# Performance work log

Hardware: AMD Instinct MI355X
Metric: run time of the kernel (lower is better)

## Reference

```python
import jax, jax.numpy as jnp
import numpy as np

N = 100000   # nodes
E = 1600000  # edges
C = 128      # channels
EPS = 1e-5   # BatchNorm eps (PyG gnn.BatchNorm default)


def gcn_conv(x, W, b, src, dst, n):
    """PyG GCNConv: linear -> sym-normalized aggregation with self-loops -> bias."""
    h = x @ W                                      # [N, C]
    # degree with self-loops: in-degree at dst + 1
    deg = jnp.zeros((n,), h.dtype).at[dst].add(jnp.ones((), h.dtype)) + 1.0
    dinv = jax.lax.rsqrt(deg)                      # [N]
    norm = dinv[src] * dinv[dst]                   # [E]
    agg = jnp.zeros_like(h).at[dst].add(h[src] * norm[:, None])
    agg = agg + h * (dinv * dinv)[:, None]         # self-loop contribution
    return agg + b


def batch_norm(x, gamma, beta):
    """Training-mode BatchNorm over the node dimension (per-channel)."""
    mu = jnp.mean(x, axis=0)
    var = jnp.mean(jnp.square(x - mu), axis=0)     # biased variance
    return (x - mu) * jax.lax.rsqrt(var + EPS) * gamma + beta


def setup_inputs() -> dict:
    key = jax.random.key(0)
    ks = jax.random.split(key, 8)
    s = 1.0 / np.sqrt(C)
    x = jax.random.normal(ks[0], (N, C), dtype=jnp.float32)
    edge_index = jax.random.randint(ks[1], (2, E), 0, N, dtype=jnp.int64)
    W1 = jax.random.uniform(ks[2], (C, C), jnp.float32, -s, s)
    b1 = jax.random.uniform(ks[3], (C,), jnp.float32, -s, s)
    W2 = jax.random.uniform(ks[4], (C, C), jnp.float32, -s, s)
    b2 = jax.random.uniform(ks[5], (C,), jnp.float32, -s, s)
    gamma2 = jnp.ones((C,), jnp.float32)
    beta2 = jnp.zeros((C,), jnp.float32)
    return {"x": x, "W1": W1, "b1": b1, "W2": W2, "b2": b2,
            "gamma2": gamma2, "beta2": beta2, "edge_index": edge_index}


def reference(x, W1, b1, W2, b2, gamma2, beta2, edge_index):
    src, dst = edge_index[0], edge_index[1]
    identity = x
    # NOTE: original forward applies batch_norm2 after BOTH convs (batch_norm1 unused).
    h = jax.nn.relu(batch_norm(gcn_conv(x, W1, b1, src, dst, N), gamma2, beta2))
    h = batch_norm(gcn_conv(h, W2, b2, src, dst, N), gamma2, beta2)
    return jax.nn.relu(h + identity)
```

## Files before the change

kernel.cpp:

```cpp
#include <hip/hip_runtime.h>

#define N_NODES 100000
#define EDGES   1600000
#define CH      128
#define BN_EPS  1e-5f

#define BINS     782
#define CHUNKS   256
#define CHUNK_E  (EDGES / CHUNKS)
#define HM       (BINS * CHUNKS)
#define SCAN_NB  (HM / 256)
#define NREP     64

typedef __attribute__((ext_vector_type(8))) __bf16 bf16x8;
typedef __attribute__((ext_vector_type(4))) __bf16 bf16x4;
typedef __attribute__((ext_vector_type(2))) __bf16 bf16x2;
typedef __attribute__((ext_vector_type(4))) float  f32x4;

__global__ __launch_bounds__(256) void histo_kernel(const int* __restrict__ dst,
                                                    int* __restrict__ histo_g) {
    __shared__ int h[BINS];
    int t = threadIdx.x;
    for (int b = t; b < BINS; b += 256) h[b] = 0;
    __syncthreads();
    int base = blockIdx.x * CHUNK_E;
    for (int i = t; i < CHUNK_E; i += 256)
        atomicAdd(&h[dst[base + i] >> 7], 1);
    __syncthreads();
    for (int b = t; b < BINS; b += 256)
        histo_g[b * CHUNKS + blockIdx.x] = h[b];
}

__global__ __launch_bounds__(256) void scan1(const int* __restrict__ in,
                                             int* __restrict__ scanned,
                                             int* __restrict__ blocksum) {
    __shared__ int sh[2][256];
    int t = threadIdx.x;
    int i = blockIdx.x * 256 + t;
    int v = in[i];
    sh[0][t] = v;
    __syncthreads();
    int pp = 0;
    #pragma unroll
    for (int off = 1; off < 256; off <<= 1) {
        int val = sh[pp][t] + ((t >= off) ? sh[pp][t - off] : 0);
        sh[1 - pp][t] = val;
        pp = 1 - pp;
        __syncthreads();
    }
    int incl = sh[pp][t];
    scanned[i] = incl - v;
    if (t == 255) blocksum[blockIdx.x] = incl;
}

__global__ __launch_bounds__(1024) void scan2(int* __restrict__ blocksum) {
    __shared__ int sh[2][1024];
    int t = threadIdx.x;
    int v = (t < SCAN_NB) ? blocksum[t] : 0;
    sh[0][t] = v;
    __syncthreads();
    int pp = 0;
    #pragma unroll
    for (int off = 1; off < 1024; off <<= 1) {
        int val = sh[pp][t] + ((t >= off) ? sh[pp][t - off] : 0);
        sh[1 - pp][t] = val;
        pp = 1 - pp;
        __syncthreads();
    }
    if (t < SCAN_NB) blocksum[t] = sh[pp][t] - v;
}

__global__ __launch_bounds__(256) void place_kernel(const int* __restrict__ src,
                                                    const int* __restrict__ dst,
                                                    const int* __restrict__ scanned,
                                                    const int* __restrict__ blocksum,
                                                    int* __restrict__ binned) {
    __shared__ int cur[BINS];
    int t = threadIdx.x;
    for (int b = t; b < BINS; b += 256)
        cur[b] = scanned[b * CHUNKS + blockIdx.x] + blocksum[b];
    __syncthreads();
    int base = blockIdx.x * CHUNK_E;
    for (int i = t; i < CHUNK_E; i += 256) {
        int d = dst[base + i];
        int s = src[base + i];
        int pos = atomicAdd(&cur[d >> 7], 1);
        binned[pos] = (s << 7) | (d & 127);
    }
}

__global__ __launch_bounds__(256) void bin_csr(const int* __restrict__ binned,
                                               const int* __restrict__ scanned,
                                               const int* __restrict__ blocksum,
                                               int* __restrict__ srcs,
                                               int* __restrict__ rowptr,
                                               float* __restrict__ dinv) {
    __shared__ int cnt[128];
    __shared__ int sc[2][128];
    __shared__ int base[128];
    __shared__ int cur[128];
    const int t = threadIdx.x;
    const int bin = blockIdx.x;
    if (t < 128) { cnt[t] = 0; cur[t] = 0; }
    __syncthreads();
    const int beg = scanned[bin * CHUNKS] + blocksum[bin];
    const int end = (bin == BINS - 1) ? EDGES
                    : (scanned[(bin + 1) * CHUNKS] + blocksum[bin + 1]);
    for (int e = beg + t; e < end; e += 256)
        atomicAdd(&cnt[binned[e] & 127], 1);
    __syncthreads();
    if (t < 128) sc[0][t] = cnt[t];
    __syncthreads();
    int pp = 0;
    #pragma unroll
    for (int off = 1; off < 128; off <<= 1) {
        if (t < 128) sc[1 - pp][t] = sc[pp][t] + ((t >= off) ? sc[pp][t - off] : 0);
        pp = 1 - pp;
        __syncthreads();
    }
    if (t < 128) {
        base[t] = beg + sc[pp][t] - cnt[t];
        int n = (bin << 7) + t;
        if (n < N_NODES) {
            rowptr[n] = base[t];
            dinv[n] = rsqrtf((float)cnt[t] + 1.0f);
        }
    }
    if (bin == 0 && t == 0) rowptr[N_NODES] = EDGES;
    __syncthreads();
    for (int e = beg + t; e < end; e += 256) {
        int p = binned[e];
        int dl = p & 127;
        int pos = base[dl] + atomicAdd(&cur[dl], 1);
        srcs[pos] = p >> 7;
    }
}

__global__ __launch_bounds__(256) void wtrans2(const float* __restrict__ W1,
                                               __bf16* __restrict__ Wt1,
                                               const float* __restrict__ W2,
                                               __bf16* __restrict__ Wt2,
                                               unsigned* __restrict__ hspad) {
    int b = blockIdx.x;
    if (b == 0 && threadIdx.x < 64) hspad[threadIdx.x] = 0u;
    const float* W = (b < 64) ? W1 : W2;
    __bf16* Wt = (b < 64) ? Wt1 : Wt2;
    int idx = (b & 63) * 256 + threadIdx.x;
    int n = idx >> 7, k = idx & 127;
    Wt[idx] = (__bf16)W[k * 128 + n];
}

__global__ __launch_bounds__(256) void gemm_f32(const float* __restrict__ A,
                                                const __bf16* __restrict__ Wt,
                                                const float* __restrict__ dinv,
                                                __bf16* __restrict__ hs) {
    const int wave = threadIdx.x >> 6;
    const int rt = blockIdx.x * 4 + wave;
    if (rt >= N_NODES / 16) return;
    const int lane = threadIdx.x & 63;
    const int ln = lane & 15;
    const int quad = lane >> 4;
    const int arow = rt * 16 + ln;

    f32x4 acc[8];
    #pragma unroll
    for (int ct = 0; ct < 8; ++ct) acc[ct] = (f32x4){0.f, 0.f, 0.f, 0.f};

    #pragma unroll
    for (int k0 = 0; k0 < 128; k0 += 32) {
        const int k = k0 + quad * 8;
        float4 a0 = *(const float4*)(A + (size_t)arow * CH + k);
        float4 a1 = *(const float4*)(A + (size_t)arow * CH + k + 4);
        bf16x8 af;
        af[0] = (__bf16)a0.x; af[1] = (__bf16)a0.y;
        af[2] = (__bf16)a0.z; af[3] = (__bf16)a0.w;
        af[4] = (__bf16)a1.x; af[5] = (__bf16)a1.y;
        af[6] = (__bf16)a1.z; af[7] = (__bf16)a1.w;
        #pragma unroll
        for (int ct = 0; ct < 8; ++ct) {
            bf16x8 bfrag = *(const bf16x8*)(Wt + (size_t)(ct * 16 + ln) * CH + k);
            acc[ct] = __builtin_amdgcn_mfma_f32_16x16x32_bf16(af, bfrag, acc[ct], 0, 0, 0);
        }
    }

    #pragma unroll
    for (int r = 0; r < 4; ++r) {
        const int row_r = rt * 16 + quad * 4 + r;
        const float dr = dinv[row_r];
        __bf16* orow = hs + (size_t)row_r * CH + ln;
        #pragma unroll
        for (int ct = 0; ct < 8; ++ct)
            orow[ct * 16] = (__bf16)(acc[ct][r] * dr);
    }
}

__global__ __launch_bounds__(256) void gemm_bn(const __bf16* __restrict__ A,
                                               const __bf16* __restrict__ Wt,
                                               const float* __restrict__ dinv,
                                               const float* __restrict__ scale,
                                               const float* __restrict__ shift,
                                               __bf16* __restrict__ hs) {
    const int wave = threadIdx.x >> 6;
    const int rt = blockIdx.x * 4 + wave;
    if (rt >= N_NODES / 16) return;
    const int lane = threadIdx.x & 63;
    const int ln = lane & 15;
    const int quad = lane >> 4;
    const int arow = rt * 16 + ln;

    f32x4 acc[8];
    #pragma unroll
    for (int ct = 0; ct < 8; ++ct) acc[ct] = (f32x4){0.f, 0.f, 0.f, 0.f};

    #pragma unroll
    for (int k0 = 0; k0 < 128; k0 += 32) {
        const int k = k0 + quad * 8;
        bf16x8 av = *(const bf16x8*)(A + (size_t)arow * CH + k);
        bf16x8 af;
        #pragma unroll
        for (int j = 0; j < 8; ++j)
            af[j] = (__bf16)fmaxf(fmaf((float)av[j], scale[k + j], shift[k + j]), 0.f);
        #pragma unroll
        for (int ct = 0; ct < 8; ++ct) {
            bf16x8 bfrag = *(const bf16x8*)(Wt + (size_t)(ct * 16 + ln) * CH + k);
            acc[ct] = __builtin_amdgcn_mfma_f32_16x16x32_bf16(af, bfrag, acc[ct], 0, 0, 0);
        }
    }

    #pragma unroll
    for (int r = 0; r < 4; ++r) {
        const int row_r = rt * 16 + quad * 4 + r;
        const float dr = dinv[row_r];
        __bf16* orow = hs + (size_t)row_r * CH + ln;
        #pragma unroll
        for (int ct = 0; ct < 8; ++ct)
            orow[ct * 16] = (__bf16)(acc[ct][r] * dr);
    }
}

__global__ __launch_bounds__(256) void gather_agg(const __bf16* __restrict__ hs,
                                                  const int* __restrict__ srcs,
                                                  const int* __restrict__ rowptr,
                                                  const float* __restrict__ dinv,
                                                  __bf16* __restrict__ agg,
                                                  float* __restrict__ gpart) {
    __shared__ float red[4][64][4];
    const int wave = threadIdx.x >> 6;
    const int c2 = threadIdx.x & 63;
    const bf16x2* hp = (const bf16x2*)hs;

    const int n0 = __builtin_amdgcn_readfirstlane(blockIdx.x * 8 + wave * 2);
    const int n1 = n0 + 1;
    const int b0 = rowptr[n0];
    const int e0 = rowptr[n0 + 1];
    const int e1 = rowptr[n1 + 1];
    const int b1 = e0;
    const int d0 = e0 - b0, d1 = e1 - b1;
    const int nt = (max(d0, d1) + 7) >> 3;

    bf16x2 sv0 = hp[(size_t)n0 * 64 + c2];
    bf16x2 sv1 = hp[(size_t)n1 * 64 + c2];
    float ax0 = (float)sv0[0], ay0 = (float)sv0[1];
    float ax1 = (float)sv1[0], ay1 = (float)sv1[1];

    int j0 = b0, j1 = b1;
    for (int t = 0; t < nt; ++t) {
        int ea[8], eb[8];
        #pragma unroll
        for (int u = 0; u < 8; ++u) {
            int sa = srcs[j0 + u];
            int sb = srcs[j1 + u];
            ea[u] = (j0 + u < e0) ? sa : N_NODES;
            eb[u] = (j1 + u < e1) ? sb : N_NODES;
        }
        bf16x2 va[8], vb[8];
        #pragma unroll
        for (int u = 0; u < 8; ++u) va[u] = hp[(size_t)ea[u] * 64 + c2];
        #pragma unroll
        for (int u = 0; u < 8; ++u) vb[u] = hp[(size_t)eb[u] * 64 + c2];
        ax0 += (((float)va[0][0] + (float)va[1][0]) + ((float)va[2][0] + (float)va[3][0]))
             + (((float)va[4][0] + (float)va[5][0]) + ((float)va[6][0] + (float)va[7][0]));
        ay0 += (((float)va[0][1] + (float)va[1][1]) + ((float)va[2][1] + (float)va[3][1]))
             + (((float)va[4][1] + (float)va[5][1]) + ((float)va[6][1] + (float)va[7][1]));
        ax1 += (((float)vb[0][0] + (float)vb[1][0]) + ((float)vb[2][0] + (float)vb[3][0]))
             + (((float)vb[4][0] + (float)vb[5][0]) + ((float)vb[6][0] + (float)vb[7][0]));
        ay1 += (((float)vb[0][1] + (float)vb[1][1]) + ((float)vb[2][1] + (float)vb[3][1]))
             + (((float)vb[4][1] + (float)vb[5][1]) + ((float)vb[6][1] + (float)vb[7][1]));
        j0 += 8; j1 += 8;
    }

    const float dd0 = dinv[n0], dd1 = dinv[n1];
    const float o0x = ax0 * dd0, o0y = ay0 * dd0;
    const float o1x = ax1 * dd1, o1y = ay1 * dd1;
    bf16x2 o0; o0[0] = (__bf16)o0x; o0[1] = (__bf16)o0y;
    bf16x2 o1; o1[0] = (__bf16)o1x; o1[1] = (__bf16)o1y;
    ((bf16x2*)agg)[(size_t)n0 * 64 + c2] = o0;
    ((bf16x2*)agg)[(size_t)n1 * 64 + c2] = o1;

    f32x4 rv;
    rv[0] = o0x + o1x; rv[1] = o0x * o0x + o1x * o1x;
    rv[2] = o0y + o1y; rv[3] = o0y * o0y + o1y * o1y;
    *(f32x4*)red[wave][c2] = rv;
    __syncthreads();
    const int t = threadIdx.x;
    float v = red[0][t >> 2][t & 3] + red[1][t >> 2][t & 3] +
              red[2][t >> 2][t & 3] + red[3][t >> 2][t & 3];
    atomicAdd(&gpart[(blockIdx.x & (NREP - 1)) * 256 + t], v);
}

__global__ __launch_bounds__(1024) void bn_final(const float* __restrict__ gpart,
                                                 const float* __restrict__ gamma,
                                                 const float* __restrict__ beta,
                                                 float* __restrict__ scale,
                                                 float* __restrict__ shift) {
    int t = threadIdx.x;
    int c  = t >> 3;
    int rg = t & 7;
    int c2 = c >> 1, odd = c & 1;
    int slot = c2 * 4 + 2 * odd;
    float s = 0.f, ss = 0.f;
    #pragma unroll
    for (int k = 0; k < NREP; k += 8) {
        s  += gpart[(rg + k) * 256 + slot];
        ss += gpart[(rg + k) * 256 + slot + 1];
    }
    s  += __shfl_xor(s, 1);  ss += __shfl_xor(ss, 1);
    s  += __shfl_xor(s, 2);  ss += __shfl_xor(ss, 2);
    s  += __shfl_xor(s, 4);  ss += __shfl_xor(ss, 4);
    if (rg == 0) {
        const float invN = 1.0f / (float)N_NODES;
        float mu = s * invN;
        float var = ss * invN - mu * mu;
        float sc = gamma[c] * rsqrtf(var + BN_EPS);
        scale[c] = sc;
        shift[c] = beta[c] - mu * sc;
    }
}

__global__ __launch_bounds__(256) void bn_apply_res_relu(const __bf16* __restrict__ v,
                                                         const float* __restrict__ scale,
                                                         const float* __restrict__ shift,
                                                         const float* __restrict__ xin,
                                                         float* __restrict__ outv) {
    int i = blockIdx.x * 256 + threadIdx.x;
    int cg = i & 31;
    bf16x4 a4 = ((const bf16x4*)v)[i];
    float4 r = ((const float4*)xin)[i];
    float4 sc = ((const float4*)scale)[cg];
    float4 sh = ((const float4*)shift)[cg];
    float4 a;
    a.x = fmaxf(fmaf((float)a4[0], sc.x, sh.x) + r.x, 0.f);
    a.y = fmaxf(fmaf((float)a4[1], sc.y, sh.y) + r.y, 0.f);
    a.z = fmaxf(fmaf((float)a4[2], sc.z, sh.z) + r.z, 0.f);
    a.w = fmaxf(fmaf((float)a4[3], sc.w, sh.w) + r.w, 0.f);
    ((float4*)outv)[i] = a;
}

extern "C" void kernel_launch(void* const* d_in, const int* in_sizes, int n_in,
                              void* d_out, int out_size, void* d_ws, size_t ws_size,
                              hipStream_t stream) {
    const float* x      = (const float*)d_in[0];
    const float* W1     = (const float*)d_in[1];
    const float* W2     = (const float*)d_in[3];
    const float* gamma2 = (const float*)d_in[5];
    const float* beta2  = (const float*)d_in[6];
    const int*   ei     = (const int*)d_in[7];
    const int*   srcI   = ei;
    const int*   dstI   = ei + EDGES;
    float* out = (float*)d_out;

    char* ws = (char*)d_ws;
    __bf16*   agg      = (__bf16*)(ws);
    __bf16*   hs       = (__bf16*)(ws + 25600000);
    unsigned* hspad    = (unsigned*)(ws + 51200000);
    int*      binned   = (int*)   (ws + 51200256);
    int*      srcs     = (int*)   (ws + 57600256);
    int*      histo_g  = (int*)   (ws + 64000256);
    int*      scanned  = (int*)   (ws + 64801024);
    int*      blocksum = (int*)   (ws + 65601792);
    float*    dinv     = (float*) (ws + 65604920);
    int*      rowptr   = (int*)   (ws + 66004920);
    __bf16*   Wt1      = (__bf16*)(ws + 66404928);
    __bf16*   Wt2      = (__bf16*)(ws + 66437696);
    float*    scale1   = (float*) (ws + 66470464);
    float*    shift1   = scale1 + 128;
    float*    scale2   = scale1 + 256;
    float*    shift2   = scale1 + 384;

    float* gpart1 = (float*)binned;
    float* gpart2 = gpart1 + NREP * 256;

    const int ELEM4_BLOCKS  = (N_NODES * 32) / 256;
    const int GEMM_BLOCKS   = (N_NODES / 16 + 3) / 4;
    const int GATHER_BLOCKS = N_NODES / 8;

    histo_kernel<<<CHUNKS, 256, 0, stream>>>(dstI, histo_g);
    scan1<<<SCAN_NB, 256, 0, stream>>>(histo_g, scanned, blocksum);
    scan2<<<1, 1024, 0, stream>>>(blocksum);
    place_kernel<<<CHUNKS, 256, 0, stream>>>(srcI, dstI, scanned, blocksum, binned);
    bin_csr<<<BINS, 256, 0, stream>>>(binned, scanned, blocksum, srcs, rowptr, dinv);
    wtrans2<<<128, 256, 0, stream>>>(W1, Wt1, W2, Wt2, hspad);
    hipMemsetAsync(gpart1, 0, 2 * NREP * 256 * sizeof(float), stream);

    gemm_f32<<<GEMM_BLOCKS, 256, 0, stream>>>(x, Wt1, dinv, hs);
    gather_agg<<<GATHER_BLOCKS, 256, 0, stream>>>(hs, srcs, rowptr, dinv, agg, gpart1);
    bn_final<<<1, 1024, 0, stream>>>(gpart1, gamma2, beta2, scale1, shift1);

    gemm_bn<<<GEMM_BLOCKS, 256, 0, stream>>>(agg, Wt2, dinv, scale1, shift1, hs);
    gather_agg<<<GATHER_BLOCKS, 256, 0, stream>>>(hs, srcs, rowptr, dinv, agg, gpart2);
    bn_final<<<1, 1024, 0, stream>>>(gpart2, gamma2, beta2, scale2, shift2);
    bn_apply_res_relu<<<ELEM4_BLOCKS, 256, 0, stream>>>(agg, scale2, shift2, x, out);
}
```

Baseline: 397.7 us.

## Replace two-level binned CSR build with direct global-atomic counting sort

Drops the bin histogram, two-pass scan, bin placement and per-bin CSR kernels. Node degrees are now counted with global atomics, scanned in a single 1024-thread block, and edges are scattered straight into CSR slots with global atomic cursors. Zeroing of the counts and BN partial buffers is folded into the weight-transpose kernel, which removes a memset. This cuts kernel launches and an intermediate pass over the edges, at the cost of contended global atomics, a serial per-thread scan loop, and a nondeterministic neighbour order inside each row.

Result: slower. 801.9 us (+101.6%).

```diff
diff --git a/kernel.cpp b/kernel.cpp
--- a/kernel.cpp
+++ b/kernel.cpp
@@ -4,60 +4,51 @@
 #define EDGES   1600000
 #define CH      128
 #define BN_EPS  1e-5f
-
-#define BINS     782
-#define CHUNKS   256
-#define CHUNK_E  (EDGES / CHUNKS)
-#define HM       (BINS * CHUNKS)
-#define SCAN_NB  (HM / 256)
-#define NREP     64
+#define NREP    64
 
 typedef __attribute__((ext_vector_type(8))) __bf16 bf16x8;
 typedef __attribute__((ext_vector_type(4))) __bf16 bf16x4;
 typedef __attribute__((ext_vector_type(2))) __bf16 bf16x2;
 typedef __attribute__((ext_vector_type(4))) float  f32x4;
 
-__global__ __launch_bounds__(256) void histo_kernel(const int* __restrict__ dst,
-                                                    int* __restrict__ histo_g) {
-    __shared__ int h[BINS];
-    int t = threadIdx.x;
-    for (int b = t; b < BINS; b += 256) h[b] = 0;
-    __syncthreads();
-    int base = blockIdx.x * CHUNK_E;
-    for (int i = t; i < CHUNK_E; i += 256)
-        atomicAdd(&h[dst[base + i] >> 7], 1);
-    __syncthreads();
-    for (int b = t; b < BINS; b += 256)
-        histo_g[b * CHUNKS + blockIdx.x] = h[b];
-}
-
-__global__ __launch_bounds__(256) void scan1(const int* __restrict__ in,
-                                             int* __restrict__ scanned,
-                                             int* __restrict__ blocksum) {
-    __shared__ int sh[2][256];
-    int t = threadIdx.x;
-    int i = blockIdx.x * 256 + t;
-    int v = in[i];
-    sh[0][t] = v;
-    __syncthreads();
-    int pp = 0;
-    #pragma unroll
-    for (int off = 1; off < 256; off <<= 1) {
-        int val = sh[pp][t] + ((t >= off) ? sh[pp][t - off] : 0);
-        sh[1 - pp][t] = val;
-        pp = 1 - pp;
-        __syncthreads();
-    }
-    int incl = sh[pp][t];
-    scanned[i] = incl - v;
-    if (t == 255) blocksum[blockIdx.x] = incl;
-}
-
-__global__ __launch_bounds__(1024) void scan2(int* __restrict__ blocksum) {
+__global__ __launch_bounds__(256) void wtrans2z(const float* __restrict__ W1,
+                                                __bf16* __restrict__ Wt1,
+                                                const float* __restrict__ W2,
+                                                __bf16* __restrict__ Wt2,
+                                                unsigned* __restrict__ hspad,
+                                                int* __restrict__ cnt,
+                                                float* __restrict__ gpart) {
+    int tid = blockIdx.x * 256 + threadIdx.x;
+    if (tid < 64) hspad[tid] = 0u;
+    gpart[tid] = 0.f;
+    for (int i = tid; i < N_NODES; i += 32768) cnt[i] = 0;
+    int b = blockIdx.x;
+    const float* W = (b < 64) ? W1 : W2;
+    __bf16* Wt = (b < 64) ? Wt1 : Wt2;
+    int idx = (b & 63) * 256 + threadIdx.x;
+    int n = idx >> 7, k = idx & 127;
+    Wt[idx] = (__bf16)W[k * 128 + n];
+}
+
+__global__ __launch_bounds__(256) void count_deg(const int* __restrict__ dst,
+                                                 int* __restrict__ cnt) {
+    int base = blockIdx.x * 2560 + threadIdx.x;
+    #pragma unroll
+    for (int u = 0; u < 10; ++u)
+        atomicAdd(&cnt[dst[base + u * 256]], 1);
+}
+
+__global__ __launch_bounds__(1024) void scan_deg(const int* __restrict__ cnt,
+                                                 int* __restrict__ rowptr,
+                                                 int* __restrict__ cur,
+                                                 float* __restrict__ dinv) {
     __shared__ int sh[2][1024];
-    int t = threadIdx.x;
-    int v = (t < SCAN_NB) ? blocksum[t] : 0;
-    sh[0][t] = v;
+    const int t = threadIdx.x;
+    const int lo = t * 98;
+    const int hi = min(lo + 98, N_NODES);
+    int s = 0;
+    for (int i = lo; i < hi; ++i) s += cnt[i];
+    sh[0][t] = s;
     __syncthreads();
     int pp = 0;
     #pragma unroll
@@ -67,87 +58,30 @@
         pp = 1 - pp;
         __syncthreads();
     }
-    if (t < SCAN_NB) blocksum[t] = sh[pp][t] - v;
-}
-
-__global__ __launch_bounds__(256) void place_kernel(const int* __restrict__ src,
+    int run = sh[pp][t] - s;
+    for (int i = lo; i < hi; ++i) {
+        int c = cnt[i];
+        rowptr[i] = run;
+        cur[i] = run;
+        dinv[i] = rsqrtf((float)c + 1.0f);
+        run += c;
+    }
+    if (t == 0) rowptr[N_NODES] = EDGES;
+}
+
+__global__ __launch_bounds__(256) void place_direct(const int* __restrict__ src,
                                                     const int* __restrict__ dst,
-                                                    const int* __restrict__ scanned,
-                                                    const int* __restrict__ blocksum,
-                                                    int* __restrict__ binned) {
-    __shared__ int cur[BINS];
-    int t = threadIdx.x;
-    for (int b = t; b < BINS; b += 256)
-        cur[b] = scanned[b * CHUNKS + blockIdx.x] + blocksum[b];
-    __syncthreads();
-    int base = blockIdx.x * CHUNK_E;
-    for (int i = t; i < CHUNK_E; i += 256) {
-        int d = dst[base + i];
-        int s = src[base + i];
-        int pos = atomicAdd(&cur[d >> 7], 1);
-        binned[pos] = (s << 7) | (d & 127);
-    }
-}
-
-__global__ __launch_bounds__(256) void bin_csr(const int* __restrict__ binned,
-                                               const int* __restrict__ scanned,
-                                               const int* __restrict__ blocksum,
-                                               int* __restrict__ srcs,
-                                               int* __restrict__ rowptr,
-                                               float* __restrict__ dinv) {
-    __shared__ int cnt[128];
-    __shared__ int sc[2][128];
-    __shared__ int base[128];
-    __shared__ int cur[128];
-    const int t = threadIdx.x;
-    const int bin = blockIdx.x;
-    if (t < 128) { cnt[t] = 0; cur[t] = 0; }
-    __syncthreads();
-    const int beg = scanned[bin * CHUNKS] + blocksum[bin];
-    const int end = (bin == BINS - 1) ? EDGES
-                    : (scanned[(bin + 1) * CHUNKS] + blocksum[bin + 1]);
-    for (int e = beg + t; e < end; e += 256)
-        atomicAdd(&cnt[binned[e] & 127], 1);
-    __syncthreads();
-    if (t < 128) sc[0][t] = cnt[t];
-    __syncthreads();
-    int pp = 0;
-    #pragma unroll
-    for (int off = 1; off < 128; off <<= 1) {
-        if (t < 128) sc[1 - pp][t] = sc[pp][t] + ((t >= off) ? sc[pp][t - off] : 0);
-        pp = 1 - pp;
-        __syncthreads();
-    }
-    if (t < 128) {
-        base[t] = beg + sc[pp][t] - cnt[t];
-        int n = (bin << 7) + t;
-        if (n < N_NODES) {
-            rowptr[n] = base[t];
-            dinv[n] = rsqrtf((float)cnt[t] + 1.0f);
-        }
-    }
-    if (bin == 0 && t == 0) rowptr[N_NODES] = EDGES;
-    __syncthreads();
-    for (int e = beg + t; e < end; e += 256) {
-        int p = binned[e];
-        int dl = p & 127;
-        int pos = base[dl] + atomicAdd(&cur[dl], 1);
-        srcs[pos] = p >> 7;
-    }
-}
-
-__global__ __launch_bounds__(256) void wtrans2(const float* __restrict__ W1,
-                                               __bf16* __restrict__ Wt1,
-                                               const float* __restrict__ W2,
-                                               __bf16* __restrict__ Wt2,
-                                               unsigned* __restrict__ hspad) {
-    int b = blockIdx.x;
-    if (b == 0 && threadIdx.x < 64) hspad[threadIdx.x] = 0u;
-    const float* W = (b < 64) ? W1 : W2;
-    __bf16* Wt = (b < 64) ? Wt1 : Wt2;
-    int idx = (b & 63) * 256 + threadIdx.x;
-    int n = idx >> 7, k = idx & 127;
-    Wt[idx] = (__bf16)W[k * 128 + n];
+                                                    int* __restrict__ cur,
+                                                    int* __restrict__ srcs) {
+    int base = blockIdx.x * 2560 + threadIdx.x;
+    #pragma unroll
+    for (int u = 0; u < 10; ++u) {
+        int e = base + u * 256;
+        int d = dst[e];
+        int s = src[e];
+        int pos = atomicAdd(&cur[d], 1);
+        srcs[pos] = s;
+    }
 }
 
 __global__ __launch_bounds__(256) void gemm_f32(const float* __restrict__ A,
@@ -370,37 +304,32 @@
     float* out = (float*)d_out;
 
     char* ws = (char*)d_ws;
-    __bf16*   agg      = (__bf16*)(ws);
-    __bf16*   hs       = (__bf16*)(ws + 25600000);
-    unsigned* hspad    = (unsigned*)(ws + 51200000);
-    int*      binned   = (int*)   (ws + 51200256);
-    int*      srcs     = (int*)   (ws + 57600256);
-    int*      histo_g  = (int*)   (ws + 64000256);
-    int*      scanned  = (int*)   (ws + 64801024);
-    int*      blocksum = (int*)   (ws + 65601792);
-    float*    dinv     = (float*) (ws + 65604920);
-    int*      rowptr   = (int*)   (ws + 66004920);
-    __bf16*   Wt1      = (__bf16*)(ws + 66404928);
-    __bf16*   Wt2      = (__bf16*)(ws + 66437696);
-    float*    scale1   = (float*) (ws + 66470464);
-    float*    shift1   = scale1 + 128;
-    float*    scale2   = scale1 + 256;
-    float*    shift2   = scale1 + 384;
-
-    float* gpart1 = (float*)binned;
-    float* gpart2 = gpart1 + NREP * 256;
+    __bf16*   agg    = (__bf16*)(ws);
+    __bf16*   hs     = (__bf16*)(ws + 25600000);
+    unsigned* hspad  = (unsigned*)(ws + 51200000);
+    int*      srcs   = (int*)   (ws + 51200256);
+    int*      cnt    = (int*)   (ws + 57600256);
+    int*      rowptr = (int*)   (ws + 58000256);
+    int*      cur    = (int*)   (ws + 58400260);
+    float*    dinv   = (float*) (ws + 58800260);
+    __bf16*   Wt1    = (__bf16*)(ws + 59200260);
+    __bf16*   Wt2    = (__bf16*)(ws + 59233028);
+    float*    gpart1 = (float*) (ws + 59265796);
+    float*    gpart2 = gpart1 + NREP * 256;
+    float*    scale1 = (float*) (ws + 59396868);
+    float*    shift1 = scale1 + 128;
+    float*    scale2 = scale1 + 256;
+    float*    shift2 = scale1 + 384;
 
     const int ELEM4_BLOCKS  = (N_NODES * 32) / 256;
     const int GEMM_BLOCKS   = (N_NODES / 16 + 3) / 4;
     const int GATHER_BLOCKS = N_NODES / 8;
-
-    histo_kernel<<<CHUNKS, 256, 0, stream>>>(dstI, histo_g);
-    scan1<<<SCAN_NB, 256, 0, stream>>>(histo_g, scanned, blocksum);
-    scan2<<<1, 1024, 0, stream>>>(blocksum);
-    place_kernel<<<CHUNKS, 256, 0, stream>>>(srcI, dstI, scanned, blocksum, binned);
-    bin_csr<<<BINS, 256, 0, stream>>>(binned, scanned, blocksum, srcs, rowptr, dinv);
-    wtrans2<<<128, 256, 0, stream>>>(W1, Wt1, W2, Wt2, hspad);
-    hipMemsetAsync(gpart1, 0, 2 * NREP * 256 * sizeof(float), stream);
+    const int EDGE_BLOCKS   = EDGES / 2560;
+
+    wtrans2z<<<128, 256, 0, stream>>>(W1, Wt1, W2, Wt2, hspad, cnt, gpart1);
+    count_deg<<<EDGE_BLOCKS, 256, 0, stream>>>(dstI, cnt);
+    scan_deg<<<1, 1024, 0, stream>>>(cnt, rowptr, cur, dinv);
+    place_direct<<<EDGE_BLOCKS, 256, 0, stream>>>(srcI, dstI, cur, srcs);
 
     gemm_f32<<<GEMM_BLOCKS, 256, 0, stream>>>(x, Wt1, dinv, hs);
     gather_agg<<<GATHER_BLOCKS, 256, 0, stream>>>(hs, srcs, rowptr, dinv, agg, gpart1);
```
